# Kernel tuning notes

Measured on AMD Instinct MI355X. Metric: run time of the kernel, lower is better.

The kernel has to match this reference:

```python
import jax, jax.numpy as jnp
import numpy as np

B, L, H, NH, NB = 16, 200, 128, 2, 2
ITEMS, SPAN = 50000, 256
NEG = -2.0**32 + 1.0  # mask value used by the torch module


def _ln(x, g, b, eps=1e-8):
    m = jnp.mean(x, axis=-1, keepdims=True)
    v = jnp.mean((x - m) ** 2, axis=-1, keepdims=True)
    return (x - m) / jnp.sqrt(v + eps) * g + b


def setup_inputs() -> dict:
    key = jax.random.key(0)
    ks = jax.random.split(key, 20)
    p = lambda k, s: (jax.random.normal(k, s, jnp.float32) * 0.02)
    item_emb = p(ks[0], (ITEMS + 1, H)).at[0].set(0.0)  # padding_idx=0
    return {
        "user_ids": jax.random.randint(ks[1], (B,), 0, 10000),
        "log_seqs": jax.random.randint(ks[2], (B, L), 0, ITEMS),
        "time_matrices": jax.random.randint(ks[3], (B, L, L), 0, SPAN),
        "pos_seqs": jax.random.randint(ks[4], (B, L), 0, ITEMS),
        "neg_seqs": jax.random.randint(ks[5], (B, L), 0, ITEMS),
        "item_emb": item_emb,
        "pos_K_emb": p(ks[6], (L, H)),
        "pos_V_emb": p(ks[7], (L, H)),
        "time_K_emb": p(ks[8], (SPAN + 1, H)),
        "time_V_emb": p(ks[9], (SPAN + 1, H)),
        "Wq": p(ks[10], (NB, H, H)), "bq": jnp.zeros((NB, H)),
        "Wk": p(ks[11], (NB, H, H)), "bk": jnp.zeros((NB, H)),
        "Wv": p(ks[12], (NB, H, H)), "bv": jnp.zeros((NB, H)),
        "ln1_g": jnp.ones((NB, H)), "ln1_b": jnp.zeros((NB, H)),
        "W1": p(ks[13], (NB, H, H)), "b1": jnp.zeros((NB, H)),
        "W2": p(ks[14], (NB, H, H)), "b2": jnp.zeros((NB, H)),
        "ln2_g": jnp.ones((NB, H)), "ln2_b": jnp.zeros((NB, H)),
        "lnf_g": jnp.ones((H,)), "lnf_b": jnp.zeros((H,)),
    }


def reference(user_ids, log_seqs, time_matrices, pos_seqs, neg_seqs,
              item_emb, pos_K_emb, pos_V_emb, time_K_emb, time_V_emb,
              Wq, bq, Wk, bk, Wv, bv, ln1_g, ln1_b,
              W1, b1, W2, b2, ln2_g, ln2_b, lnf_g, lnf_b):
    d = H // NH
    pad = (log_seqs == 0)                    # (B,L) timeline mask
    keep = (~pad)[..., None].astype(jnp.float32)

    seqs = item_emb[log_seqs] * jnp.sqrt(jnp.float32(H))
    seqs = seqs * keep
    posK = pos_K_emb.reshape(L, NH, d)       # same for every batch element
    posV = pos_V_emb.reshape(L, NH, d)
    tmK = time_K_emb[time_matrices].reshape(B, L, L, NH, d)  # (B,L,L,h,d)
    tmV = time_V_emb[time_matrices].reshape(B, L, L, NH, d)
    causal = ~jnp.tril(jnp.ones((L, L), dtype=bool))          # True = masked
    mask = pad[:, None, :, None] | causal[None, None, :, :]   # (B,1,L,L) row-mask | causal

    for i in range(NB):
        Q = (seqs @ Wq[i].T + bq[i]).reshape(B, L, NH, d)
        K = (seqs @ Wk[i].T + bk[i]).reshape(B, L, NH, d)
        V = (seqs @ Wv[i].T + bv[i]).reshape(B, L, NH, d)
        aw = jnp.einsum('bqhd,bkhd->bhqk', Q, K)
        aw = aw + jnp.einsum('bqhd,khd->bhqk', Q, posK)
        aw = aw + jnp.einsum('bqkhd,bqhd->bhqk', tmK, Q)
        aw = aw / jnp.sqrt(jnp.float32(d))
        aw = jnp.where(mask, NEG, aw)
        A = jax.nn.softmax(aw, axis=-1)                        # (B,h,L,L)
        out = jnp.einsum('bhqk,bkhd->bqhd', A, V)
        out = out + jnp.einsum('bhqk,khd->bqhd', A, posV)
        out = out + jnp.einsum('bhqk,bqkhd->bqhd', A, tmV)
        out = out.reshape(B, L, H)
        seqs = _ln(seqs + out, ln1_g[i], ln1_b[i])
        ffn = jax.nn.relu(seqs @ W1[i].T + b1[i]) @ W2[i].T + b2[i]
        seqs = _ln(seqs + ffn, ln2_g[i], ln2_b[i])
        seqs = seqs * keep

    log_feats = _ln(seqs, lnf_g, lnf_b)
    pos_logits = jnp.sum(log_feats * item_emb[pos_seqs], axis=-1)  # (B,L)
    neg_logits = jnp.sum(log_feats * item_emb[neg_seqs], axis=-1)
    return jnp.stack([pos_logits, neg_logits])  # (2,B,L)
```

## Files before the change

### kernel.cpp

```cpp
#include <hip/hip_runtime.h>
#include <hip/hip_bf16.h>
#include <math.h>

#define BB 16
#define LL 200
#define HH 128
#define DD 64
#define NQT 25
#define NEGF -4294967295.0f
#define SQRTH 11.313708498984761f

__global__ __launch_bounds__(256) void k_prep(const float* __restrict__ Wq,
    const float* __restrict__ Wk, const float* __restrict__ Wv,
    const float* __restrict__ W1, const float* __restrict__ W2,
    float* __restrict__ WT) {
    int m = blockIdx.x >> 4, tile = blockIdx.x & 15;
    const float* base = (m < 2) ? Wq : (m < 4) ? Wk : (m < 6) ? Wv : (m < 8) ? W1 : W2;
    const float* src = base + (m & 1) * HH * HH;
    float* dst = WT + m * HH * HH;
    __shared__ float tb[32][33];
    int t = threadIdx.x;
    int tr = tile >> 2, tc = tile & 3;
    int lr = t >> 3, lc = (t & 7) * 4;
    float4 v = *(const float4*)(src + (tr * 32 + lr) * HH + tc * 32 + lc);
    tb[lr][lc + 0] = v.x; tb[lr][lc + 1] = v.y;
    tb[lr][lc + 2] = v.z; tb[lr][lc + 3] = v.w;
    __syncthreads();
    float4 o;
    o.x = tb[lc + 0][lr]; o.y = tb[lc + 1][lr];
    o.z = tb[lc + 2][lr]; o.w = tb[lc + 3][lr];
    *(float4*)(dst + (tc * 32 + lr) * HH + tr * 32 + lc) = o;
}

__global__ __launch_bounds__(256) void k_qkv(float* __restrict__ seqs,
    const int* __restrict__ log_seqs, const float* __restrict__ item_emb, int do_embed,
    const float* __restrict__ WTq, const float* __restrict__ bq,
    const float* __restrict__ WTk, const float* __restrict__ bk,
    const float* __restrict__ WTv, const float* __restrict__ bv,
    const float* __restrict__ posK, const float* __restrict__ posV,
    float* __restrict__ Q, float* __restrict__ Kp, float* __restrict__ Vp) {
    __shared__ float s_lds[8][HH];
    int r0g = blockIdx.x * 8;
    int t = threadIdx.x;
    {
        int r = t >> 5, d4 = t & 31;
        if (do_embed) {
            int id = log_seqs[r0g + r];
            float4 v = make_float4(0.f, 0.f, 0.f, 0.f);
            if (id != 0) {
                v = ((const float4*)(item_emb + id * HH))[d4];
                v.x *= SQRTH; v.y *= SQRTH; v.z *= SQRTH; v.w *= SQRTH;
            }
            *(float4*)&s_lds[r][d4 * 4] = v;
            ((float4*)(seqs + r0g * HH))[t] = v;
        } else {
            ((float4*)s_lds)[t] = ((const float4*)(seqs + r0g * HH))[t];
        }
    }
    __syncthreads();
    int r = t >> 5, j = t & 31;
    const float4* wq4 = (const float4*)WTq + j;
    const float4* wk4 = (const float4*)WTk + j;
    const float4* wv4 = (const float4*)WTv + j;
    float4 aq = make_float4(0.f, 0.f, 0.f, 0.f);
    float4 ak = make_float4(0.f, 0.f, 0.f, 0.f);
    float4 av = make_float4(0.f, 0.f, 0.f, 0.f);
#pragma unroll 4
    for (int k = 0; k < HH; ++k) {
        float sv = s_lds[r][k];
        float4 wq = wq4[k * 32];
        float4 wk = wk4[k * 32];
        float4 wv = wv4[k * 32];
        aq.x += sv * wq.x; aq.y += sv * wq.y; aq.z += sv * wq.z; aq.w += sv * wq.w;
        ak.x += sv * wk.x; ak.y += sv * wk.y; ak.z += sv * wk.z; ak.w += sv * wk.w;
        av.x += sv * wv.x; av.y += sv * wv.y; av.z += sv * wv.z; av.w += sv * wv.w;
    }
    int row = r0g + r;
    int l = row % LL;
    {
        float4 b = ((const float4*)bq)[j];
        aq.x += b.x; aq.y += b.y; aq.z += b.z; aq.w += b.w;
        ((float4*)(Q + row * HH))[j] = aq;
    }
    {
        float4 b = ((const float4*)bk)[j];
        float4 p = ((const float4*)(posK + l * HH))[j];
        ak.x += b.x + p.x; ak.y += b.y + p.y; ak.z += b.z + p.z; ak.w += b.w + p.w;
        ((float4*)(Kp + row * HH))[j] = ak;
    }
    {
        float4 b = ((const float4*)bv)[j];
        float4 p = ((const float4*)(posV + l * HH))[j];
        av.x += b.x + p.x; av.y += b.y + p.y; av.z += b.z + p.z; av.w += b.w + p.w;
        ((float4*)(Vp + row * HH))[j] = av;
    }
}

__global__ __launch_bounds__(256) void k_proj(const float* __restrict__ Q,
    const float* __restrict__ timeK, float* __restrict__ projK) {
    int bh = blockIdx.x / 25, qt = blockIdx.x % 25;
    int b = bh >> 1, h = bh & 1;
    int qlo = qt * 8;
    __shared__ float Qs[8][68];
    __shared__ float TK[32][68];
    int t = threadIdx.x;
    if (t < 128) {
        int r = t >> 4, d4 = t & 15;
        *(float4*)&Qs[r][d4 * 4] =
            ((const float4*)(Q + (b * LL + qlo + r) * HH + h * DD))[d4];
    }
    int tq = t >> 5, ttl = t & 31;
    for (int ch = 0; ch < 9; ++ch) {
        int base = ch * 32;
        __syncthreads();
        for (int x = t; x < 512; x += 256) {
            int i = x >> 4, d4 = x & 15;
            int tt = base + i;
            if (tt < 257)
                *(float4*)&TK[i][d4 * 4] =
                    ((const float4*)(timeK + tt * HH + h * DD))[d4];
        }
        __syncthreads();
        int tt = base + ttl;
        if (tt < 257) {
            float acc = 0.f;
#pragma unroll
            for (int d4 = 0; d4 < 16; ++d4) {
                float4 qv = *(const float4*)&Qs[tq][d4 * 4];
                float4 kv = *(const float4*)&TK[ttl][d4 * 4];
                acc += qv.x * kv.x + qv.y * kv.y + qv.z * kv.z + qv.w * kv.w;
            }
            projK[(bh * LL + qlo + tq) * 257 + tt] = acc;
        }
    }
}

__global__ __launch_bounds__(256) void k_attn(
    const float* __restrict__ Q, const float* __restrict__ Kp, const float* __restrict__ Vp,
    const float* __restrict__ projK, const float* __restrict__ timeV,
    const int* __restrict__ tm, const int* __restrict__ log_seqs,
    float* __restrict__ attnout) {
    int bh = blockIdx.x / NQT, qt = blockIdx.x % NQT;
    int b = bh >> 1, h = bh & 1;
    int qlo = qt * 8;
    __shared__ float K_s[32][68];
    __shared__ float smemW[457 * 12];
    __shared__ int s_allmask;
#define WT(i, j) smemW[(i) * 12 + (j)]
    int t = threadIdx.x;
    int tq = t >> 5, lane = t & 31, g = tq;
    int q = qlo + tq;
    int qhi = qlo + 7;

    if (t == 0) s_allmask = 0;
    for (int x = 200 * 12 + t; x < 457 * 12; x += 256) smemW[x] = 0.f;
    float4 qreg[16];
    {
        const float4* qp = (const float4*)(Q + (b * LL + q) * HH + h * DD);
#pragma unroll
        for (int d4 = 0; d4 < 16; ++d4) qreg[d4] = qp[d4];
    }
    const int* tmrow = tm + (b * LL + q) * LL;
    const float* projrow = projK + (bh * LL + q) * 257;
    const int* lsrow = log_seqs + b * LL;

    float s[7];
#pragma unroll
    for (int j = 0; j < 7; ++j) s[j] = NEGF;
    int nkc = (qhi >> 5) + 1;
#pragma unroll
    for (int kc = 0; kc < 7; ++kc) {
        if (kc < nkc) {
            int kbase = kc * 32;
            for (int x = t; x < 512; x += 256) {
                int i = x >> 4, d4 = x & 15;
                int k = kbase + i;
                if (k < LL)
                    *(float4*)&K_s[i][d4 * 4] =
                        ((const float4*)(Kp + (b * LL + k) * HH + h * DD))[d4];
            }
            __syncthreads();
            int k = kbase + lane;
            if (k <= q && lsrow[k] != 0) {
                float acc = 0.f;
#pragma unroll
                for (int d4 = 0; d4 < 16; ++d4) {
                    float4 kv = *(const float4*)&K_s[lane][d4 * 4];
                    acc += qreg[d4].x * kv.x + qreg[d4].y * kv.y +
                           qreg[d4].z * kv.z + qreg[d4].w * kv.w;
                }
                s[kc] = (acc + projrow[tmrow[k]]) * 0.125f;
            }
            __syncthreads();
        }
    }

    float mx = s[0];
#pragma unroll
    for (int j = 1; j < 7; ++j) mx = fmaxf(mx, s[j]);
    mx = fmaxf(mx, __shfl_xor(mx, 1, 64));
    mx = fmaxf(mx, __shfl_xor(mx, 2, 64));
    mx = fmaxf(mx, __shfl_xor(mx, 4, 64));
    mx = fmaxf(mx, __shfl_xor(mx, 8, 64));
    mx = fmaxf(mx, __shfl_xor(mx, 16, 64));
    bool allmask = (mx == NEGF);
    float sum = 0.f;
#pragma unroll
    for (int j = 0; j < 7; ++j) {
        int k = lane + 32 * j;
        float e = (k < LL) ? __expf(s[j] - mx) : 0.f;
        s[j] = e;
        sum += e;
    }
    sum += __shfl_xor(sum, 1, 64);
    sum += __shfl_xor(sum, 2, 64);
    sum += __shfl_xor(sum, 4, 64);
    sum += __shfl_xor(sum, 8, 64);
    sum += __shfl_xor(sum, 16, 64);
    float inv = 1.0f / sum;
    int klim = allmask ? LL : (q + 1);
    if (allmask && lane == 0) s_allmask = 1;
#pragma unroll
    for (int j = 0; j < 7; ++j) {
        int k = lane + 32 * j;
        if (k < LL) {
            float p = s[j] * inv;
            WT(k, tq) = p;
            if (k < klim && p != 0.f)
                atomicAdd(&WT(200 + tmrow[k], tq), p);
        }
    }
    __syncthreads();

    int kmax = s_allmask ? LL : (qhi + 1);
    float a00=0.f,a01=0.f,a10=0.f,a11=0.f,a20=0.f,a21=0.f,a30=0.f,a31=0.f;
    float a40=0.f,a41=0.f,a50=0.f,a51=0.f,a60=0.f,a61=0.f,a70=0.f,a71=0.f;
#define PV_STEP(WROW, SRCPTR)                                            \
    {                                                                    \
        const float* wr = &WROW;                                         \
        float4 w0 = *(const float4*)wr;                                  \
        float4 w1 = *(const float4*)(wr + 4);                            \
        float2 vv = *(const float2*)(SRCPTR);                            \
        a00 += w0.x * vv.x; a01 += w0.x * vv.y;                          \
        a10 += w0.y * vv.x; a11 += w0.y * vv.y;                          \
        a20 += w0.z * vv.x; a21 += w0.z * vv.y;                          \
        a30 += w0.w * vv.x; a31 += w0.w * vv.y;                          \
        a40 += w1.x * vv.x; a41 += w1.x * vv.y;                          \
        a50 += w1.y * vv.x; a51 += w1.y * vv.y;                          \
        a60 += w1.z * vv.x; a61 += w1.z * vv.y;                          \
        a70 += w1.w * vv.x; a71 += w1.w * vv.y;                          \
    }
    for (int i = g; i < kmax; i += 8)
        PV_STEP(WT(i, 0), Vp + (b * LL + i) * HH + h * DD + lane * 2);
    for (int i = g; i < 257; i += 8)
        PV_STEP(WT(200 + i, 0), timeV + i * HH + h * DD + lane * 2);
#undef PV_STEP
    __syncthreads();
    float* part = smemW;
    part[g * 512 + 0 * 64 + lane * 2] = a00; part[g * 512 + 0 * 64 + lane * 2 + 1] = a01;
    part[g * 512 + 1 * 64 + lane * 2] = a10; part[g * 512 + 1 * 64 + lane * 2 + 1] = a11;
    part[g * 512 + 2 * 64 + lane * 2] = a20; part[g * 512 + 2 * 64 + lane * 2 + 1] = a21;
    part[g * 512 + 3 * 64 + lane * 2] = a30; part[g * 512 + 3 * 64 + lane * 2 + 1] = a31;
    part[g * 512 + 4 * 64 + lane * 2] = a40; part[g * 512 + 4 * 64 + lane * 2 + 1] = a41;
    part[g * 512 + 5 * 64 + lane * 2] = a50; part[g * 512 + 5 * 64 + lane * 2 + 1] = a51;
    part[g * 512 + 6 * 64 + lane * 2] = a60; part[g * 512 + 6 * 64 + lane * 2 + 1] = a61;
    part[g * 512 + 7 * 64 + lane * 2] = a70; part[g * 512 + 7 * 64 + lane * 2 + 1] = a71;
    __syncthreads();
    {
        float ox = 0.f, oy = 0.f;
#pragma unroll
        for (int gg = 0; gg < 8; ++gg) {
            ox += part[gg * 512 + tq * 64 + lane * 2];
            oy += part[gg * 512 + tq * 64 + lane * 2 + 1];
        }
        *(float2*)(attnout + (b * LL + q) * HH + h * DD + lane * 2) =
            make_float2(ox, oy);
    }
#undef WT
}

__global__ __launch_bounds__(256) void k_ffn(
    float* __restrict__ seqs, const float* __restrict__ AO,
    const float* __restrict__ g1, const float* __restrict__ be1,
    const float* __restrict__ WT1, const float* __restrict__ b1,
    const float* __restrict__ WT2, const float* __restrict__ b2,
    const float* __restrict__ g2, const float* __restrict__ be2,
    const int* __restrict__ log_seqs, int do_final,
    const float* __restrict__ lnf_g, const float* __restrict__ lnf_b,
    const float* __restrict__ item_emb,
    const int* __restrict__ pos_seqs, const int* __restrict__ neg_seqs,
    float* __restrict__ out) {
    __shared__ float s_lds[8][HH];
    __shared__ float h_lds[8][HH];
    int r0g = blockIdx.x * 8;
    int t = threadIdx.x;
    {
        float4 a = ((const float4*)(seqs + r0g * HH))[t];
        float4 o = ((const float4*)(AO + r0g * HH))[t];
        a.x += o.x; a.y += o.y; a.z += o.z; a.w += o.w;
        ((float4*)s_lds)[t] = a;
    }
    __syncthreads();
    int w = t >> 6, lane = t & 63;
    int lrow = w * 2 + (lane >> 5), cl = lane & 31;
    {
        float sm = 0.f;
#pragma unroll
        for (int j = 0; j < 4; ++j) sm += s_lds[lrow][cl + 32 * j];
        sm += __shfl_xor(sm, 1, 64);  sm += __shfl_xor(sm, 2, 64);
        sm += __shfl_xor(sm, 4, 64);  sm += __shfl_xor(sm, 8, 64);
        sm += __shfl_xor(sm, 16, 64);
        float mean = sm * (1.0f / HH);
        float vr = 0.f;
#pragma unroll
        for (int j = 0; j < 4; ++j) {
            float d = s_lds[lrow][cl + 32 * j] - mean;
            vr += d * d;
        }
        vr += __shfl_xor(vr, 1, 64);  vr += __shfl_xor(vr, 2, 64);
        vr += __shfl_xor(vr, 4, 64);  vr += __shfl_xor(vr, 8, 64);
        vr += __shfl_xor(vr, 16, 64);
        float rstd = rsqrtf(vr * (1.0f / HH) + 1e-8f);
#pragma unroll
        for (int j = 0; j < 4; ++j) {
            int c = cl + 32 * j;
            s_lds[lrow][c] = (s_lds[lrow][c] - mean) * rstd * g1[c] + be1[c];
        }
    }
    __syncthreads();
    int r = t >> 5, j = t & 31;
    {
        const float4* w4 = (const float4*)WT1 + j;
        float4 acc = make_float4(0.f, 0.f, 0.f, 0.f);
#pragma unroll 4
        for (int k = 0; k < HH; ++k) {
            float sv = s_lds[r][k];
            float4 ww = w4[k * 32];
            acc.x += sv * ww.x; acc.y += sv * ww.y;
            acc.z += sv * ww.z; acc.w += sv * ww.w;
        }
        float4 b = ((const float4*)b1)[j];
        acc.x = fmaxf(acc.x + b.x, 0.f); acc.y = fmaxf(acc.y + b.y, 0.f);
        acc.z = fmaxf(acc.z + b.z, 0.f); acc.w = fmaxf(acc.w + b.w, 0.f);
        *(float4*)&h_lds[r][j * 4] = acc;
    }
    __syncthreads();
    float4 x2;
    {
        const float4* w4 = (const float4*)WT2 + j;
        float4 acc = make_float4(0.f, 0.f, 0.f, 0.f);
#pragma unroll 4
        for (int k = 0; k < HH; ++k) {
            float hv = h_lds[r][k];
            float4 ww = w4[k * 32];
            acc.x += hv * ww.x; acc.y += hv * ww.y;
            acc.z += hv * ww.z; acc.w += hv * ww.w;
        }
        float4 b = ((const float4*)b2)[j];
        float4 s1 = *(const float4*)&s_lds[r][j * 4];
        x2.x = s1.x + acc.x + b.x; x2.y = s1.y + acc.y + b.y;
        x2.z = s1.z + acc.z + b.z; x2.w = s1.w + acc.w + b.w;
    }
    __syncthreads();
    *(float4*)&h_lds[r][j * 4] = x2;
    __syncthreads();
    {
        float sm = 0.f;
#pragma unroll
        for (int jj = 0; jj < 4; ++jj) sm += h_lds[lrow][cl + 32 * jj];
        sm += __shfl_xor(sm, 1, 64);  sm += __shfl_xor(sm, 2, 64);
        sm += __shfl_xor(sm, 4, 64);  sm += __shfl_xor(sm, 8, 64);
        sm += __shfl_xor(sm, 16, 64);
        float mean = sm * (1.0f / HH);
        float vr = 0.f;
#pragma unroll
        for (int jj = 0; jj < 4; ++jj) {
            float d = h_lds[lrow][cl + 32 * jj] - mean;
            vr += d * d;
        }
        vr += __shfl_xor(vr, 1, 64);  vr += __shfl_xor(vr, 2, 64);
        vr += __shfl_xor(vr, 4, 64);  vr += __shfl_xor(vr, 8, 64);
        vr += __shfl_xor(vr, 16, 64);
        float rstd = rsqrtf(vr * (1.0f / HH) + 1e-8f);
        int row = r0g + lrow;
        float keep = (log_seqs[row] != 0) ? 1.0f : 0.0f;
        float y2[4];
#pragma unroll
        for (int jj = 0; jj < 4; ++jj) {
            int cc = cl + 32 * jj;
            y2[jj] = ((h_lds[lrow][cc] - mean) * rstd * g2[cc] + be2[cc]) * keep;
        }
        if (!do_final) {
#pragma unroll
            for (int jj = 0; jj < 4; ++jj)
                seqs[row * HH + cl + 32 * jj] = y2[jj];
        } else {
            float sm2 = y2[0] + y2[1] + y2[2] + y2[3];
            sm2 += __shfl_xor(sm2, 1, 64);  sm2 += __shfl_xor(sm2, 2, 64);
            sm2 += __shfl_xor(sm2, 4, 64);  sm2 += __shfl_xor(sm2, 8, 64);
            sm2 += __shfl_xor(sm2, 16, 64);
            float mean2 = sm2 * (1.0f / HH);
            float vr2 = 0.f;
#pragma unroll
            for (int jj = 0; jj < 4; ++jj) {
                float d = y2[jj] - mean2;
                vr2 += d * d;
            }
            vr2 += __shfl_xor(vr2, 1, 64);  vr2 += __shfl_xor(vr2, 2, 64);
            vr2 += __shfl_xor(vr2, 4, 64);  vr2 += __shfl_xor(vr2, 8, 64);
            vr2 += __shfl_xor(vr2, 16, 64);
            float rstd2 = rsqrtf(vr2 * (1.0f / HH) + 1e-8f);
            int pid = pos_seqs[row];
            int nid = neg_seqs[row];
            float pp = 0.f, nn = 0.f;
#pragma unroll
            for (int jj = 0; jj < 4; ++jj) {
                int cc = cl + 32 * jj;
                float lf = (y2[jj] - mean2) * rstd2 * lnf_g[cc] + lnf_b[cc];
                pp += lf * item_emb[pid * HH + cc];
                nn += lf * item_emb[nid * HH + cc];
            }
            pp += __shfl_xor(pp, 1, 64);  pp += __shfl_xor(pp, 2, 64);
            pp += __shfl_xor(pp, 4, 64);  pp += __shfl_xor(pp, 8, 64);
            pp += __shfl_xor(pp, 16, 64);
            nn += __shfl_xor(nn, 1, 64);  nn += __shfl_xor(nn, 2, 64);
            nn += __shfl_xor(nn, 4, 64);  nn += __shfl_xor(nn, 8, 64);
            nn += __shfl_xor(nn, 16, 64);
            if (cl == 0) {
                out[row] = pp;
                out[BB * LL + row] = nn;
            }
        }
    }
}

extern "C" void kernel_launch(void* const* d_in, const int* in_sizes, int n_in,
                              void* d_out, int out_size, void* d_ws, size_t ws_size,
                              hipStream_t stream) {
    const int* log_seqs = (const int*)d_in[1];
    const int* tm       = (const int*)d_in[2];
    const int* pos_seqs = (const int*)d_in[3];
    const int* neg_seqs = (const int*)d_in[4];
    const float* item_emb = (const float*)d_in[5];
    const float* posK   = (const float*)d_in[6];
    const float* posV   = (const float*)d_in[7];
    const float* timeK  = (const float*)d_in[8];
    const float* timeV  = (const float*)d_in[9];
    const float* Wq = (const float*)d_in[10];
    const float* bq = (const float*)d_in[11];
    const float* Wk = (const float*)d_in[12];
    const float* bk = (const float*)d_in[13];
    const float* Wv = (const float*)d_in[14];
    const float* bv = (const float*)d_in[15];
    const float* ln1_g = (const float*)d_in[16];
    const float* ln1_b = (const float*)d_in[17];
    const float* W1 = (const float*)d_in[18];
    const float* b1 = (const float*)d_in[19];
    const float* W2 = (const float*)d_in[20];
    const float* b2 = (const float*)d_in[21];
    const float* ln2_g = (const float*)d_in[22];
    const float* ln2_b = (const float*)d_in[23];
    const float* lnf_g = (const float*)d_in[24];
    const float* lnf_b = (const float*)d_in[25];

    float* ws    = (float*)d_ws;
    float* seqs  = ws;
    float* Qb    = seqs + 409600;
    float* Kpb   = Qb + 409600;
    float* Vpb   = Kpb + 409600;
    float* AO    = Vpb + 409600;
    float* projK = AO + 409600;
    float* WT    = projK + 1644800;

    k_prep<<<160, 256, 0, stream>>>(Wq, Wk, Wv, W1, W2, WT);

    for (int i = 0; i < 2; ++i) {
        const float* WTq = WT + (0 * 2 + i) * HH * HH;
        const float* WTk = WT + (1 * 2 + i) * HH * HH;
        const float* WTv = WT + (2 * 2 + i) * HH * HH;
        const float* WT1 = WT + (3 * 2 + i) * HH * HH;
        const float* WT2 = WT + (4 * 2 + i) * HH * HH;
        k_qkv<<<BB * LL / 8, 256, 0, stream>>>(seqs, log_seqs, item_emb,
            (i == 0) ? 1 : 0,
            WTq, bq + i * HH, WTk, bk + i * HH, WTv, bv + i * HH,
            posK, posV, Qb, Kpb, Vpb);
        k_proj<<<32 * NQT, 256, 0, stream>>>(Qb, timeK, projK);
        k_attn<<<32 * NQT, 256, 0, stream>>>(Qb, Kpb, Vpb, projK, timeV,
                                             tm, log_seqs, AO);
        k_ffn<<<BB * LL / 8, 256, 0, stream>>>(seqs, AO,
            ln1_g + i * HH, ln1_b + i * HH,
            WT1, b1 + i * HH, WT2, b2 + i * HH,
            ln2_g + i * HH, ln2_b + i * HH, log_seqs,
            (i == 1) ? 1 : 0, lnf_g, lnf_b, item_emb,
            pos_seqs, neg_seqs, (float*)d_out);
    }
}
```

Baseline: 194.8 us.

## Fold weight-transpose prep into QKV kernel and read untransposed Q/K/V weights

Removes the separate k_prep launch. The QKV kernel now reads Wq/Wk/Wv rows directly, so no transpose is needed: each thread owns one output column and accumulates dot products over 4 rows of a 16-row tile, with 512 threads per block. The W1/W2 transposes run as extra blocks appended to the first-layer QKV launch, which saves one kernel launch and the Q/K/V transpose traffic. In exchange, each thread reads a weight row with a stride of HH floats, which may coalesce worse, and the grid is halved to 200 blocks.

```diff
diff --git a/kernel.cpp b/kernel.cpp
--- a/kernel.cpp
+++ b/kernel.cpp
@@ -10,89 +10,80 @@
 #define NEGF -4294967295.0f
 #define SQRTH 11.313708498984761f
 
-__global__ __launch_bounds__(256) void k_prep(const float* __restrict__ Wq,
-    const float* __restrict__ Wk, const float* __restrict__ Wv,
-    const float* __restrict__ W1, const float* __restrict__ W2,
+__global__ __launch_bounds__(512) void k_qkv(float* __restrict__ seqs,
+    const int* __restrict__ log_seqs, const float* __restrict__ item_emb, int do_embed,
+    const float* __restrict__ Wq, const float* __restrict__ bq,
+    const float* __restrict__ Wk, const float* __restrict__ bk,
+    const float* __restrict__ Wv, const float* __restrict__ bv,
+    const float* __restrict__ posK, const float* __restrict__ posV,
+    float* __restrict__ Q, float* __restrict__ Kp, float* __restrict__ Vp,
+    const float* __restrict__ W1all, const float* __restrict__ W2all,
     float* __restrict__ WT) {
-    int m = blockIdx.x >> 4, tile = blockIdx.x & 15;
-    const float* base = (m < 2) ? Wq : (m < 4) ? Wk : (m < 6) ? Wv : (m < 8) ? W1 : W2;
-    const float* src = base + (m & 1) * HH * HH;
-    float* dst = WT + m * HH * HH;
+    __shared__ float s_lds[16][HH];
     __shared__ float tb[32][33];
     int t = threadIdx.x;
-    int tr = tile >> 2, tc = tile & 3;
-    int lr = t >> 3, lc = (t & 7) * 4;
-    float4 v = *(const float4*)(src + (tr * 32 + lr) * HH + tc * 32 + lc);
-    tb[lr][lc + 0] = v.x; tb[lr][lc + 1] = v.y;
-    tb[lr][lc + 2] = v.z; tb[lr][lc + 3] = v.w;
-    __syncthreads();
-    float4 o;
-    o.x = tb[lc + 0][lr]; o.y = tb[lc + 1][lr];
-    o.z = tb[lc + 2][lr]; o.w = tb[lc + 3][lr];
-    *(float4*)(dst + (tc * 32 + lr) * HH + tr * 32 + lc) = o;
-}
-
-__global__ __launch_bounds__(256) void k_qkv(float* __restrict__ seqs,
-    const int* __restrict__ log_seqs, const float* __restrict__ item_emb, int do_embed,
-    const float* __restrict__ WTq, const float* __restrict__ bq,
-    const float* __restrict__ WTk, const float* __restrict__ bk,
-    const float* __restrict__ WTv, const float* __restrict__ bv,
-    const float* __restrict__ posK, const float* __restrict__ posV,
-    float* __restrict__ Q, float* __restrict__ Kp, float* __restrict__ Vp) {
-    __shared__ float s_lds[8][HH];
-    int r0g = blockIdx.x * 8;
-    int t = threadIdx.x;
-    {
+    if (blockIdx.x >= 200) {
+        int bid = blockIdx.x - 200;
+        int m = bid >> 4, tile = bid & 15;
+        const float* src = (m < 2) ? (W1all + m * HH * HH) : (W2all + (m - 2) * HH * HH);
+        float* dst = WT + m * HH * HH;
+        int tr = tile >> 2, tc = tile & 3;
+        if (t < 256) {
+            int lr = t >> 3, lc = (t & 7) * 4;
+            float4 v = *(const float4*)(src + (tr * 32 + lr) * HH + tc * 32 + lc);
+            tb[lr][lc + 0] = v.x; tb[lr][lc + 1] = v.y;
+            tb[lr][lc + 2] = v.z; tb[lr][lc + 3] = v.w;
+        }
+        __syncthreads();
+        if (t < 256) {
+            int lr = t >> 3, lc = (t & 7) * 4;
+            float4 o;
+            o.x = tb[lc + 0][lr]; o.y = tb[lc + 1][lr];
+            o.z = tb[lc + 2][lr]; o.w = tb[lc + 3][lr];
+            *(float4*)(dst + (tc * 32 + lr) * HH + tr * 32 + lc) = o;
+        }
+        return;
+    }
+    int r0g = blockIdx.x * 16;
+    if (do_embed) {
         int r = t >> 5, d4 = t & 31;
-        if (do_embed) {
-            int id = log_seqs[r0g + r];
-            float4 v = make_float4(0.f, 0.f, 0.f, 0.f);
-            if (id != 0) {
-                v = ((const float4*)(item_emb + id * HH))[d4];
-                v.x *= SQRTH; v.y *= SQRTH; v.z *= SQRTH; v.w *= SQRTH;
-            }
-            *(float4*)&s_lds[r][d4 * 4] = v;
-            ((float4*)(seqs + r0g * HH))[t] = v;
-        } else {
-            ((float4*)s_lds)[t] = ((const float4*)(seqs + r0g * HH))[t];
-        }
-    }
-    __syncthreads();
-    int r = t >> 5, j = t & 31;
-    const float4* wq4 = (const float4*)WTq + j;
-    const float4* wk4 = (const float4*)WTk + j;
-    const float4* wv4 = (const float4*)WTv + j;
-    float4 aq = make_float4(0.f, 0.f, 0.f, 0.f);
-    float4 ak = make_float4(0.f, 0.f, 0.f, 0.f);
-    float4 av = make_float4(0.f, 0.f, 0.f, 0.f);
+        int id = log_seqs[r0g + r];
+        float4 v = make_float4(0.f, 0.f, 0.f, 0.f);
+        if (id != 0) {
+            v = ((const float4*)(item_emb + id * HH))[d4];
+            v.x *= SQRTH; v.y *= SQRTH; v.z *= SQRTH; v.w *= SQRTH;
+        }
+        *(float4*)&s_lds[r][d4 * 4] = v;
+        ((float4*)(seqs + r0g * HH))[t] = v;
+    } else {
+        ((float4*)s_lds)[t] = ((const float4*)(seqs + r0g * HH))[t];
+    }
+    __syncthreads();
+    int c = t & 127, rg = t >> 7;
+    float aq[4] = {0.f, 0.f, 0.f, 0.f};
+    float ak[4] = {0.f, 0.f, 0.f, 0.f};
+    float av[4] = {0.f, 0.f, 0.f, 0.f};
+    const float4* wq4 = (const float4*)(Wq + c * HH);
+    const float4* wk4 = (const float4*)(Wk + c * HH);
+    const float4* wv4 = (const float4*)(Wv + c * HH);
 #pragma unroll 4
-    for (int k = 0; k < HH; ++k) {
-        float sv = s_lds[r][k];
-        float4 wq = wq4[k * 32];
-        float4 wk = wk4[k * 32];
-        float4 wv = wv4[k * 32];
-        aq.x += sv * wq.x; aq.y += sv * wq.y; aq.z += sv * wq.z; aq.w += sv * wq.w;
-        ak.x += sv * wk.x; ak.y += sv * wk.y; ak.z += sv * wk.z; ak.w += sv * wk.w;
-        av.x += sv * wv.x; av.y += sv * wv.y; av.z += sv * wv.z; av.w += sv * wv.w;
-    }
-    int row = r0g + r;
-    int l = row % LL;
-    {
-        float4 b = ((const float4*)bq)[j];
-        aq.x += b.x; aq.y += b.y; aq.z += b.z; aq.w += b.w;
-        ((float4*)(Q + row * HH))[j] = aq;
-    }
-    {
-        float4 b = ((const float4*)bk)[j];
-        float4 p = ((const float4*)(posK + l * HH))[j];
-        ak.x += b.x + p.x; ak.y += b.y + p.y; ak.z += b.z + p.z; ak.w += b.w + p.w;
-        ((float4*)(Kp + row * HH))[j] = ak;
-    }
-    {
-        float4 b = ((const float4*)bv)[j];
-        float4 p = ((const float4*)(posV + l * HH))[j];
-        av.x += b.x + p.x; av.y += b.y + p.y; av.z += b.z + p.z; av.w += b.w + p.w;
-        ((float4*)(Vp + row * HH))[j] = av;
+    for (int k4 = 0; k4 < HH / 4; ++k4) {
+        float4 wq = wq4[k4], wk = wk4[k4], wv = wv4[k4];
+#pragma unroll
+        for (int r = 0; r < 4; ++r) {
+            float4 s = *(const float4*)&s_lds[rg * 4 + r][k4 * 4];
+            aq[r] += s.x * wq.x + s.y * wq.y + s.z * wq.z + s.w * wq.w;
+            ak[r] += s.x * wk.x + s.y * wk.y + s.z * wk.z + s.w * wk.w;
+            av[r] += s.x * wv.x + s.y * wv.y + s.z * wv.z + s.w * wv.w;
+        }
+    }
+#pragma unroll
+    for (int r = 0; r < 4; ++r) {
+        int row = r0g + rg * 4 + r;
+        int l = row % LL;
+        Q[row * HH + c]  = aq[r] + bq[c];
+        Kp[row * HH + c] = ak[r] + bk[c] + posK[l * HH + c];
+        Vp[row * HH + c] = av[r] + bv[c] + posV[l * HH + c];
     }
 }
 
@@ -472,18 +463,15 @@
     float* projK = AO + 409600;
     float* WT    = projK + 1644800;
 
-    k_prep<<<160, 256, 0, stream>>>(Wq, Wk, Wv, W1, W2, WT);
-
     for (int i = 0; i < 2; ++i) {
-        const float* WTq = WT + (0 * 2 + i) * HH * HH;
-        const float* WTk = WT + (1 * 2 + i) * HH * HH;
-        const float* WTv = WT + (2 * 2 + i) * HH * HH;
-        const float* WT1 = WT + (3 * 2 + i) * HH * HH;
-        const float* WT2 = WT + (4 * 2 + i) * HH * HH;
-        k_qkv<<<BB * LL / 8, 256, 0, stream>>>(seqs, log_seqs, item_emb,
+        const float* WT1 = WT + (0 * 2 + i) * HH * HH;
+        const float* WT2 = WT + (1 * 2 + i) * HH * HH;
+        k_qkv<<<(i == 0) ? 264 : 200, 512, 0, stream>>>(seqs, log_seqs, item_emb,
             (i == 0) ? 1 : 0,
-            WTq, bq + i * HH, WTk, bk + i * HH, WTv, bv + i * HH,
-            posK, posV, Qb, Kpb, Vpb);
+            Wq + i * HH * HH, bq + i * HH,
+            Wk + i * HH * HH, bk + i * HH,
+            Wv + i * HH * HH, bv + i * HH,
+            posK, posV, Qb, Kpb, Vpb, W1, W2, WT);
         k_proj<<<32 * NQT, 256, 0, stream>>>(Qb, timeK, projK);
         k_attn<<<32 * NQT, 256, 0, stream>>>(Qb, Kpb, Vpb, projK, timeV,
                                              tm, log_seqs, AO);
```

Result: no change. 194.0 us (-0.4%).
